# Performance work log

Hardware: AMD Instinct MI355X
Metric: run time of the kernel (lower is better)

The kernel has to match this reference:

```python
import jax, jax.numpy as jnp
import numpy as np

N, F_IN, F_OUT = 8192, 256, 128
ALPHA = 0.2  # LeakyReLU negative slope
NEG_INF = -9e15


def setup_inputs() -> dict:
    key = jax.random.key(0)
    k1, k2, k3, k4 = jax.random.split(key, 4)
    h = jax.random.normal(k1, (N, F_IN), dtype=jnp.float32)
    adj = jax.random.randint(k2, (N, N), 0, 2, dtype=jnp.int32)
    # Xavier-uniform-like init (gain=1.414)
    lim_w = 1.414 * np.sqrt(6.0 / (F_IN + F_OUT))
    W = jax.random.uniform(k3, (F_IN, F_OUT), dtype=jnp.float32, minval=-lim_w, maxval=lim_w)
    lim_a = 1.414 * np.sqrt(6.0 / (2 * F_OUT + 1))
    a = jax.random.uniform(k4, (2 * F_OUT, 1), dtype=jnp.float32, minval=-lim_a, maxval=lim_a)
    return {"h": h, "adj": adj, "W": W, "a": a}


def reference(h, adj, W, a):
    # Wh: [N, F_OUT]
    Wh = h @ W
    f_out = W.shape[1]
    # The torch code builds an [N, N, 2F] concat tensor; mathematically
    # e_ij = leakyrelu(a1 . Wh_i + a2 . Wh_j), so compute via two projections.
    a1 = a[:f_out, 0]   # [F_OUT]
    a2 = a[f_out:, 0]   # [F_OUT]
    f1 = Wh @ a1        # [N]
    f2 = Wh @ a2        # [N]
    e = jax.nn.leaky_relu(f1[:, None] + f2[None, :], negative_slope=ALPHA)  # [N, N]
    e = jnp.where(adj > 0, e, NEG_INF)
    attention = jax.nn.softmax(e, axis=1)  # [N, N]; dropout p=0 (eval mode)
    h_prime = attention @ Wh               # [N, F_OUT]
    return jax.nn.elu(h_prime)
```

## Files before the change

kernel.cpp:

```cpp
#include <hip/hip_runtime.h>
#include <hip/hip_bf16.h>
#include <math.h>

typedef short short8 __attribute__((ext_vector_type(8)));
typedef float f32x4 __attribute__((ext_vector_type(4)));
typedef int i32x4 __attribute__((ext_vector_type(4)));

#define NN 8192
#define FIN 256
#define FOUT 128
#define LRELU_A 0.2f
#define L2E 1.44269504088896f

__device__ __forceinline__ short f2bf(float x) {
    unsigned u = __builtin_bit_cast(unsigned, x);
    unsigned r = (u + 0x7FFFu + ((u >> 16) & 1u)) >> 16;
    return (short)r;
}

__device__ __forceinline__ short f2bf_fast(float x) {
    return __builtin_bit_cast(short, __float2bfloat16(x));
}

__global__ __launch_bounds__(256) void k_prep(const float* __restrict__ h,
                                              const float* __restrict__ W,
                                              const float* __restrict__ a,
                                              const int* __restrict__ adj,
                                              short* __restrict__ WhT,
                                              float* __restrict__ f1,
                                              float* __restrict__ f2,
                                              unsigned* __restrict__ packed) {
    __shared__ float hs[8][FIN];
    __shared__ unsigned char nib[2048];
    const int tid = threadIdx.x;
    const int bid = blockIdx.x;

    if (bid >= NN / 8) {
        const int row = bid - NN / 8;
        const i32x4* base = (const i32x4*)(adj + (size_t)row * NN);
        #pragma unroll
        for (int q = 0; q < 8; ++q) {
            int idx = q * 256 + tid;
            i32x4 v = __builtin_nontemporal_load(base + idx);
            unsigned b = (unsigned)(v.x & 1)        | ((unsigned)(v.y & 1) << 1) |
                         ((unsigned)(v.z & 1) << 2) | ((unsigned)(v.w & 1) << 3);
            nib[idx] = (unsigned char)b;
        }
        __syncthreads();
        unsigned long long n8 = *(const unsigned long long*)&nib[tid * 8];
        unsigned w = 0;
        #pragma unroll
        for (int j = 0; j < 8; ++j)
            w |= ((unsigned)((n8 >> (8 * j)) & 0xFull)) << (4 * j);
        packed[(size_t)row * (NN / 32) + tid] = w;
        return;
    }

    const int r0 = bid * 8;
    #pragma unroll
    for (int i = 0; i < 2; ++i) {
        int f4 = tid + 256 * i;
        int row = f4 >> 6;
        int k4 = (f4 & 63) << 2;
        *(float4*)&hs[row][k4] = *(const float4*)(h + (size_t)(r0 + row) * FIN + k4);
    }
    __syncthreads();
    const int c4 = (tid & 31) * 4;
    const int row = tid >> 5;
    float acc0 = 0.f, acc1 = 0.f, acc2 = 0.f, acc3 = 0.f;
    #pragma unroll 4
    for (int k = 0; k < FIN; ++k) {
        float hv = hs[row][k];
        float4 w4 = *(const float4*)(W + (size_t)k * FOUT + c4);
        acc0 = fmaf(hv, w4.x, acc0);
        acc1 = fmaf(hv, w4.y, acc1);
        acc2 = fmaf(hv, w4.z, acc2);
        acc3 = fmaf(hv, w4.w, acc3);
    }
    const int wr = r0 + row;
    WhT[(size_t)(c4 + 0) * NN + wr] = f2bf(acc0);
    WhT[(size_t)(c4 + 1) * NN + wr] = f2bf(acc1);
    WhT[(size_t)(c4 + 2) * NN + wr] = f2bf(acc2);
    WhT[(size_t)(c4 + 3) * NN + wr] = f2bf(acc3);

    float4 a1v = *(const float4*)(a + c4);
    float4 a2v = *(const float4*)(a + FOUT + c4);
    float p1 = acc0 * a1v.x + acc1 * a1v.y + acc2 * a1v.z + acc3 * a1v.w;
    float p2 = acc0 * a2v.x + acc1 * a2v.y + acc2 * a2v.z + acc3 * a2v.w;
    #pragma unroll
    for (int m = 1; m <= 16; m <<= 1) {
        p1 += __shfl_xor(p1, m, 64);
        p2 += __shfl_xor(p2, m, 64);
    }
    if ((tid & 31) == 0) {
        f1[wr] = p1;
        f2[wr] = p2;
    }
}

__global__ __launch_bounds__(256) void k_gmax(const float* __restrict__ f2,
                                              float* __restrict__ gmax) {
    const int tid = threadIdx.x;
    float m = -1e30f;
    for (int i = tid; i < NN; i += 256) m = fmaxf(m, f2[i]);
    #pragma unroll
    for (int s = 1; s <= 32; s <<= 1) m = fmaxf(m, __shfl_xor(m, s, 64));
    __shared__ float red[4];
    if ((tid & 63) == 0) red[tid >> 6] = m;
    __syncthreads();
    if (tid == 0) gmax[0] = fmaxf(fmaxf(red[0], red[1]), fmaxf(red[2], red[3]));
}

__device__ __forceinline__ void gat_body(const short* __restrict__ lrd, unsigned m8,
                                         float4 fa, float4 fb,
                                         float c1, float c2,
                                         f32x4 acc[9], short8 ones) {
    short8 b0 = *(const short8*)(lrd + 0 * 1024);
    short8 b1 = *(const short8*)(lrd + 1 * 1024);
    short8 b2 = *(const short8*)(lrd + 2 * 1024);
    short8 b3 = *(const short8*)(lrd + 3 * 1024);
    short8 b4 = *(const short8*)(lrd + 4 * 1024);
    short8 b5 = *(const short8*)(lrd + 5 * 1024);
    short8 b6 = *(const short8*)(lrd + 6 * 1024);
    short8 b7 = *(const short8*)(lrd + 7 * 1024);

    float fv[8] = {fa.x, fa.y, fa.z, fa.w, fb.x, fb.y, fb.z, fb.w};
    short8 af;
    #pragma unroll
    for (int i = 0; i < 8; ++i) {
        float u = fv[i] + c1;
        float v = fmaf(LRELU_A, fv[i], c2);
        float p = __builtin_amdgcn_exp2f(fmaxf(u, v));
        p = (m8 & (1u << i)) ? p : 0.0f;
        af[i] = f2bf_fast(p);
    }
    acc[0] = __builtin_amdgcn_mfma_f32_16x16x32_bf16(af, b0, acc[0], 0, 0, 0);
    acc[1] = __builtin_amdgcn_mfma_f32_16x16x32_bf16(af, b1, acc[1], 0, 0, 0);
    acc[2] = __builtin_amdgcn_mfma_f32_16x16x32_bf16(af, b2, acc[2], 0, 0, 0);
    acc[3] = __builtin_amdgcn_mfma_f32_16x16x32_bf16(af, b3, acc[3], 0, 0, 0);
    acc[4] = __builtin_amdgcn_mfma_f32_16x16x32_bf16(af, b4, acc[4], 0, 0, 0);
    acc[5] = __builtin_amdgcn_mfma_f32_16x16x32_bf16(af, b5, acc[5], 0, 0, 0);
    acc[6] = __builtin_amdgcn_mfma_f32_16x16x32_bf16(af, b6, acc[6], 0, 0, 0);
    acc[7] = __builtin_amdgcn_mfma_f32_16x16x32_bf16(af, b7, acc[7], 0, 0, 0);
    acc[8] = __builtin_amdgcn_mfma_f32_16x16x32_bf16(af, ones, acc[8], 0, 0, 0);
}

#define GAT_STEP(KOFF, MC, LRD0, LRD1, BUFW)                                       \
    {                                                                              \
        const int koff_ = (KOFF);                                                  \
        float4 fa0 = *(const float4*)(lf2 + koff_);                                \
        float4 fb0 = *(const float4*)(lf2 + koff_ + 4);                            \
        float4 fa1 = *(const float4*)(lf2 + koff_ + 32);                           \
        float4 fb1 = *(const float4*)(lf2 + koff_ + 36);                           \
        unsigned m0 = (MC.x >> mshift) & 0xffu;                                    \
        unsigned m1 = (MC.y >> mshift) & 0xffu;                                    \
        const int kpm_ = (koff_ + 128 < kchunk) ? koff_ + 128 : 0;                 \
        MC = *(const uint2*)(pkrow + (kpm_ >> 5));                                 \
        const int kst_ = (koff_ + 64 < kchunk) ? koff_ + 64 : 0;                   \
        short8 r0 = *(const short8*)(g00 + kst_);                                  \
        short8 r1 = *(const short8*)(g01 + kst_);                                  \
        short8 r2 = *(const short8*)(g10 + kst_);                                  \
        short8 r3 = *(const short8*)(g11 + kst_);                                  \
        gat_body(LRD0, m0, fa0, fb0, c1, c2, acc, ones);                           \
        gat_body(LRD1, m1, fa1, fb1, c1, c2, acc, ones);                           \
        *(short8*)((BUFW) + d00) = r0;                                             \
        *(short8*)((BUFW) + d01) = r1;                                             \
        *(short8*)((BUFW) + d10) = r2;                                             \
        *(short8*)((BUFW) + d11) = r3;                                             \
        asm volatile("s_waitcnt lgkmcnt(0)" ::: "memory");                         \
        __builtin_amdgcn_s_barrier();                                              \
    }

__global__ __launch_bounds__(256, 4) void k_attn(const unsigned* __restrict__ packed,
                                                 const short* __restrict__ WhT,
                                                 const float* __restrict__ f1,
                                                 const float* __restrict__ f2,
                                                 const float* __restrict__ gmax,
                                                 float* __restrict__ numb,
                                                 float* __restrict__ denb,
                                                 int kchunk, int nsplit) {
    __shared__ __align__(16) short ldsW[2][8192];
    __shared__ __align__(16) float ldsF2[2048];
    const int tid = threadIdx.x;
    const int lane = tid & 63;
    const int wave = tid >> 6;
    const int split = blockIdx.x & (nsplit - 1);
    const int rt = blockIdx.x / nsplit;
    const int rowbase = rt * 64 + wave * 16;
    const int col = lane & 15;
    const int kg = lane >> 4;
    const int arow = rowbase + col;

    const float f1r = f1[arow];
    const float gm = gmax[0];
    const float t0v = f1r + gm;
    const float mhat = fmaxf(t0v, LRELU_A * t0v);
    const float mh2 = mhat * L2E;
    const float c1 = fmaf(f1r, L2E, -mh2);
    const float c2 = fmaf(LRELU_A * f1r, L2E, -mh2);

    const short8 ones = {0x3F80, 0x3F80, 0x3F80, 0x3F80,
                         0x3F80, 0x3F80, 0x3F80, 0x3F80};

    const int kbase0 = split * kchunk;
    const unsigned* pkrow = packed + (size_t)arow * (NN / 32) + (kbase0 >> 5);
    const int mshift = kg * 8;
    const float* lf2 = ldsF2 + kg * 8;

    const int srow = wave * 32 + (lane >> 2);
    const int sx = srow & 7;
    const short* gsb = WhT + (size_t)srow * NN + kbase0 + (lane & 3) * 8;
    const short* g00 = gsb;
    const short* g01 = gsb + 32;
    const short* g10 = gsb + (size_t)16 * NN;
    const short* g11 = gsb + (size_t)16 * NN + 32;
    const int d00 = srow * 64        + ((((lane & 3) + 0) ^ sx) * 8);
    const int d01 = srow * 64        + ((((lane & 3) + 4) ^ sx) * 8);
    const int d10 = (srow + 16) * 64 + ((((lane & 3) + 0) ^ sx) * 8);
    const int d11 = (srow + 16) * 64 + ((((lane & 3) + 4) ^ sx) * 8);
    short* buf0 = &ldsW[0][0];
    short* buf1 = &ldsW[1][0];

    const short* lrdE0 = &ldsW[0][col * 64 + ((kg ^ (col & 7)) * 8)];
    const short* lrdE1 = &ldsW[0][col * 64 + (((kg ^ (col & 7)) * 8) ^ 32)];
    const short* lrdO0 = lrdE0 + 8192;
    const short* lrdO1 = lrdE1 + 8192;

    f32x4 acc[9] = {};

    for (int i = tid * 4; i < kchunk; i += 1024) {
        float4 v = *(const float4*)(f2 + kbase0 + i);
        v.x *= L2E; v.y *= L2E; v.z *= L2E; v.w *= L2E;
        *(float4*)&ldsF2[i] = v;
    }
    {
        short8 r0 = *(const short8*)(g00);
        short8 r1 = *(const short8*)(g01);
        short8 r2 = *(const short8*)(g10);
        short8 r3 = *(const short8*)(g11);
        *(short8*)(buf0 + d00) = r0;
        *(short8*)(buf0 + d01) = r1;
        *(short8*)(buf0 + d10) = r2;
        *(short8*)(buf0 + d11) = r3;
    }
    uint2 mA = *(const uint2*)(pkrow);
    uint2 mB = *(const uint2*)(pkrow + 2);
    asm volatile("s_waitcnt lgkmcnt(0)" ::: "memory");
    __builtin_amdgcn_s_barrier();

    for (int koff = 0; koff < kchunk; koff += 128) {
        GAT_STEP(koff,      mA, lrdE0, lrdE1, buf1);
        GAT_STEP(koff + 64, mB, lrdO0, lrdO1, buf0);
    }

    const int rsub = (lane >> 4) * 4;
    if (col == 0) {
        #pragma unroll
        for (int r = 0; r < 4; ++r)
            denb[(size_t)split * NN + rowbase + rsub + r] = acc[8][r];
    }

    float* np = numb + ((size_t)split * NN + rowbase) * FOUT;
    #pragma unroll
    for (int t = 0; t < 8; ++t) {
        #pragma unroll
        for (int r = 0; r < 4; ++r) {
            np[(size_t)(rsub + r) * FOUT + t * 16 + col] = acc[t][r];
        }
    }
}

__global__ __launch_bounds__(256) void k_final(const float* __restrict__ numb,
                                               const float* __restrict__ denb,
                                               float* __restrict__ out,
                                               int splitk) {
    const int idx = blockIdx.x * 256 + threadIdx.x;
    const int row = idx >> 7;
    float s = 0.0f, d = 0.0f;
    for (int sp = 0; sp < splitk; ++sp) {
        s += numb[((size_t)sp * NN) * FOUT + idx];
        d += denb[(size_t)sp * NN + row];
    }
    float v = s / d;
    out[idx] = v > 0.0f ? v : expm1f(v);
}

extern "C" void kernel_launch(void* const* d_in, const int* in_sizes, int n_in,
                              void* d_out, int out_size, void* d_ws, size_t ws_size,
                              hipStream_t stream) {
    const float* h = (const float*)d_in[0];
    const int* adj = (const int*)d_in[1];
    const float* W = (const float*)d_in[2];
    const float* a = (const float*)d_in[3];
    float* out = (float*)d_out;

    char* ws = (char*)d_ws;
    size_t off = 0;
    auto alloc = [&](size_t nbytes) {
        char* p = ws + off;
        off = (off + nbytes + 255) & ~(size_t)255;
        return p;
    };
    short* WhT     = (short*)alloc((size_t)FOUT * NN * 2);
    float* f1      = (float*)alloc(NN * 4);
    float* f2      = (float*)alloc(NN * 4);
    float* gmx     = (float*)alloc(256);
    unsigned* pkd  = (unsigned*)alloc((size_t)NN * (NN / 32) * 4);

    int splitk = 8;
    while (splitk > 1 &&
           off + (size_t)splitk * ((size_t)NN * FOUT * 4 + NN * 4 + 512) > ws_size)
        splitk >>= 1;
    float* numb = (float*)alloc((size_t)splitk * NN * FOUT * 4);
    float* denb = (float*)alloc((size_t)splitk * NN * 4);
    const int kchunk = NN / splitk;

    k_prep<<<NN / 8 + NN, 256, 0, stream>>>(h, W, a, adj, WhT, f1, f2, pkd);
    k_gmax<<<1, 256, 0, stream>>>(f2, gmx);
    k_attn<<<(NN / 64) * splitk, 256, 0, stream>>>(pkd, WhT, f1, f2, gmx, numb, denb,
                                                   kchunk, splitk);
    k_final<<<NN * FOUT / 256, 256, 0, stream>>>(numb, denb, out, splitk);
}
```

Measured before the change: 127.1 us.

## Stream WhT tiles via direct global-to-LDS loads and prefetch f2 from global

Replaces the register-staged copy of WhT tiles into shared memory with global_load_lds direct transfers, using a new XOR swizzle on the source address. The f2 values are no longer staged in LDS; each lane prefetches its own f2 and mask values from global memory one step ahead, with the log2e scaling folded into the FMAs. Synchronisation moves from lgkmcnt waits to vmcnt counting, and the B-fragment LDS reads are split into two groups to reduce register pressure. This aims to cut VGPR use and LDS store traffic, at the cost of a fragile vmcnt count and a swizzle that must match the reader's layout.

```diff
diff --git a/kernel.cpp b/kernel.cpp
--- a/kernel.cpp
+++ b/kernel.cpp
@@ -20,6 +20,12 @@
 
 __device__ __forceinline__ short f2bf_fast(float x) {
     return __builtin_bit_cast(short, __float2bfloat16(x));
+}
+
+__device__ __forceinline__ void gload_lds16(const void* g, void* l) {
+    __builtin_amdgcn_global_load_lds(
+        (const __attribute__((address_space(1))) void*)g,
+        (__attribute__((address_space(3))) void*)l, 16, 0, 0);
 }
 
 __global__ __launch_bounds__(256) void k_prep(const float* __restrict__ h,
@@ -115,59 +121,59 @@
                                          float4 fa, float4 fb,
                                          float c1, float c2,
                                          f32x4 acc[9], short8 ones) {
-    short8 b0 = *(const short8*)(lrd + 0 * 1024);
-    short8 b1 = *(const short8*)(lrd + 1 * 1024);
-    short8 b2 = *(const short8*)(lrd + 2 * 1024);
-    short8 b3 = *(const short8*)(lrd + 3 * 1024);
-    short8 b4 = *(const short8*)(lrd + 4 * 1024);
-    short8 b5 = *(const short8*)(lrd + 5 * 1024);
-    short8 b6 = *(const short8*)(lrd + 6 * 1024);
-    short8 b7 = *(const short8*)(lrd + 7 * 1024);
-
     float fv[8] = {fa.x, fa.y, fa.z, fa.w, fb.x, fb.y, fb.z, fb.w};
     short8 af;
     #pragma unroll
     for (int i = 0; i < 8; ++i) {
-        float u = fv[i] + c1;
-        float v = fmaf(LRELU_A, fv[i], c2);
+        float u = fmaf(L2E, fv[i], c1);
+        float v = fmaf(LRELU_A * L2E, fv[i], c2);
         float p = __builtin_amdgcn_exp2f(fmaxf(u, v));
         p = (m8 & (1u << i)) ? p : 0.0f;
         af[i] = f2bf_fast(p);
     }
-    acc[0] = __builtin_amdgcn_mfma_f32_16x16x32_bf16(af, b0, acc[0], 0, 0, 0);
-    acc[1] = __builtin_amdgcn_mfma_f32_16x16x32_bf16(af, b1, acc[1], 0, 0, 0);
-    acc[2] = __builtin_amdgcn_mfma_f32_16x16x32_bf16(af, b2, acc[2], 0, 0, 0);
-    acc[3] = __builtin_amdgcn_mfma_f32_16x16x32_bf16(af, b3, acc[3], 0, 0, 0);
-    acc[4] = __builtin_amdgcn_mfma_f32_16x16x32_bf16(af, b4, acc[4], 0, 0, 0);
-    acc[5] = __builtin_amdgcn_mfma_f32_16x16x32_bf16(af, b5, acc[5], 0, 0, 0);
-    acc[6] = __builtin_amdgcn_mfma_f32_16x16x32_bf16(af, b6, acc[6], 0, 0, 0);
-    acc[7] = __builtin_amdgcn_mfma_f32_16x16x32_bf16(af, b7, acc[7], 0, 0, 0);
+    {
+        short8 b0 = *(const short8*)(lrd + 0 * 1024);
+        short8 b1 = *(const short8*)(lrd + 1 * 1024);
+        short8 b2 = *(const short8*)(lrd + 2 * 1024);
+        short8 b3 = *(const short8*)(lrd + 3 * 1024);
+        acc[0] = __builtin_amdgcn_mfma_f32_16x16x32_bf16(af, b0, acc[0], 0, 0, 0);
+        acc[1] = __builtin_amdgcn_mfma_f32_16x16x32_bf16(af, b1, acc[1], 0, 0, 0);
+        acc[2] = __builtin_amdgcn_mfma_f32_16x16x32_bf16(af, b2, acc[2], 0, 0, 0);
+        acc[3] = __builtin_amdgcn_mfma_f32_16x16x32_bf16(af, b3, acc[3], 0, 0, 0);
+    }
+    {
+        short8 b4 = *(const short8*)(lrd + 4 * 1024);
+        short8 b5 = *(const short8*)(lrd + 5 * 1024);
+        short8 b6 = *(const short8*)(lrd + 6 * 1024);
+        short8 b7 = *(const short8*)(lrd + 7 * 1024);
+        acc[4] = __builtin_amdgcn_mfma_f32_16x16x32_bf16(af, b4, acc[4], 0, 0, 0);
+        acc[5] = __builtin_amdgcn_mfma_f32_16x16x32_bf16(af, b5, acc[5], 0, 0, 0);
+        acc[6] = __builtin_amdgcn_mfma_f32_16x16x32_bf16(af, b6, acc[6], 0, 0, 0);
+        acc[7] = __builtin_amdgcn_mfma_f32_16x16x32_bf16(af, b7, acc[7], 0, 0, 0);
+    }
     acc[8] = __builtin_amdgcn_mfma_f32_16x16x32_bf16(af, ones, acc[8], 0, 0, 0);
 }
 
-#define GAT_STEP(KOFF, MC, LRD0, LRD1, BUFW)                                       \
+#define GAT_STEP(KOFF, MC, FA0, FB0, FA1, FB1, LRD0, LRD1, LDST)                   \
     {                                                                              \
         const int koff_ = (KOFF);                                                  \
-        float4 fa0 = *(const float4*)(lf2 + koff_);                                \
-        float4 fb0 = *(const float4*)(lf2 + koff_ + 4);                            \
-        float4 fa1 = *(const float4*)(lf2 + koff_ + 32);                           \
-        float4 fb1 = *(const float4*)(lf2 + koff_ + 36);                           \
-        unsigned m0 = (MC.x >> mshift) & 0xffu;                                    \
-        unsigned m1 = (MC.y >> mshift) & 0xffu;                                    \
-        const int kpm_ = (koff_ + 128 < kchunk) ? koff_ + 128 : 0;                 \
-        MC = *(const uint2*)(pkrow + (kpm_ >> 5));                                 \
+        uint2 mc_ = MC;                                                            \
+        float4 fa0_ = FA0, fb0_ = FB0, fa1_ = FA1, fb1_ = FB1;                     \
         const int kst_ = (koff_ + 64 < kchunk) ? koff_ + 64 : 0;                   \
-        short8 r0 = *(const short8*)(g00 + kst_);                                  \
-        short8 r1 = *(const short8*)(g01 + kst_);                                  \
-        short8 r2 = *(const short8*)(g10 + kst_);                                  \
-        short8 r3 = *(const short8*)(g11 + kst_);                                  \
-        gat_body(LRD0, m0, fa0, fb0, c1, c2, acc, ones);                           \
-        gat_body(LRD1, m1, fa1, fb1, c1, c2, acc, ones);                           \
-        *(short8*)((BUFW) + d00) = r0;                                             \
-        *(short8*)((BUFW) + d01) = r1;                                             \
-        *(short8*)((BUFW) + d10) = r2;                                             \
-        *(short8*)((BUFW) + d11) = r3;                                             \
-        asm volatile("s_waitcnt lgkmcnt(0)" ::: "memory");                         \
+        gload_lds16(gsrc0 + kst_,           (LDST) + 0 * 512);                     \
+        gload_lds16(gsrc0 + kst_ + 8 * NN,  (LDST) + 1 * 512);                     \
+        gload_lds16(gsrc0 + kst_ + 16 * NN, (LDST) + 2 * 512);                     \
+        gload_lds16(gsrc0 + kst_ + 24 * NN, (LDST) + 3 * 512);                     \
+        const int kpf_ = (koff_ + 128 < kchunk) ? koff_ + 128 : 0;                 \
+        MC  = *(const uint2*)(pkrow + (kpf_ >> 5));                                \
+        FA0 = *(const float4*)(f2g + kpf_);                                        \
+        FB0 = *(const float4*)(f2g + kpf_ + 4);                                    \
+        FA1 = *(const float4*)(f2g + kpf_ + 32);                                   \
+        FB1 = *(const float4*)(f2g + kpf_ + 36);                                   \
+        __builtin_amdgcn_sched_barrier(0);                                         \
+        gat_body(LRD0, (mc_.x >> mshift) & 0xffu, fa0_, fb0_, c1, c2, acc, ones);  \
+        gat_body(LRD1, (mc_.y >> mshift) & 0xffu, fa1_, fb1_, c1, c2, acc, ones);  \
+        asm volatile("s_waitcnt vmcnt(5)" ::: "memory");                           \
         __builtin_amdgcn_s_barrier();                                              \
     }
 
@@ -180,7 +186,6 @@
                                                  float* __restrict__ denb,
                                                  int kchunk, int nsplit) {
     __shared__ __align__(16) short ldsW[2][8192];
-    __shared__ __align__(16) float ldsF2[2048];
     const int tid = threadIdx.x;
     const int lane = tid & 63;
     const int wave = tid >> 6;
@@ -205,21 +210,13 @@
     const int kbase0 = split * kchunk;
     const unsigned* pkrow = packed + (size_t)arow * (NN / 32) + (kbase0 >> 5);
     const int mshift = kg * 8;
-    const float* lf2 = ldsF2 + kg * 8;
-
-    const int srow = wave * 32 + (lane >> 2);
-    const int sx = srow & 7;
-    const short* gsb = WhT + (size_t)srow * NN + kbase0 + (lane & 3) * 8;
-    const short* g00 = gsb;
-    const short* g01 = gsb + 32;
-    const short* g10 = gsb + (size_t)16 * NN;
-    const short* g11 = gsb + (size_t)16 * NN + 32;
-    const int d00 = srow * 64        + ((((lane & 3) + 0) ^ sx) * 8);
-    const int d01 = srow * 64        + ((((lane & 3) + 4) ^ sx) * 8);
-    const int d10 = (srow + 16) * 64 + ((((lane & 3) + 0) ^ sx) * 8);
-    const int d11 = (srow + 16) * 64 + ((((lane & 3) + 4) ^ sx) * 8);
-    short* buf0 = &ldsW[0][0];
-    short* buf1 = &ldsW[1][0];
+    const float* f2g = f2 + kbase0 + kg * 8;
+
+    const int sr = lane >> 3;
+    const short* gsrc0 = WhT + (size_t)(wave * 32 + sr) * NN + kbase0 +
+                         (((lane & 7) ^ sr) * 8);
+    short* ldstE = &ldsW[0][wave * 2048];
+    short* ldstO = &ldsW[1][wave * 2048];
 
     const short* lrdE0 = &ldsW[0][col * 64 + ((kg ^ (col & 7)) * 8)];
     const short* lrdE1 = &ldsW[0][col * 64 + (((kg ^ (col & 7)) * 8) ^ 32)];
@@ -228,29 +225,26 @@
 
     f32x4 acc[9] = {};
 
-    for (int i = tid * 4; i < kchunk; i += 1024) {
-        float4 v = *(const float4*)(f2 + kbase0 + i);
-        v.x *= L2E; v.y *= L2E; v.z *= L2E; v.w *= L2E;
-        *(float4*)&ldsF2[i] = v;
-    }
-    {
-        short8 r0 = *(const short8*)(g00);
-        short8 r1 = *(const short8*)(g01);
-        short8 r2 = *(const short8*)(g10);
-        short8 r3 = *(const short8*)(g11);
-        *(short8*)(buf0 + d00) = r0;
-        *(short8*)(buf0 + d01) = r1;
-        *(short8*)(buf0 + d10) = r2;
-        *(short8*)(buf0 + d11) = r3;
-    }
-    uint2 mA = *(const uint2*)(pkrow);
-    uint2 mB = *(const uint2*)(pkrow + 2);
-    asm volatile("s_waitcnt lgkmcnt(0)" ::: "memory");
+    gload_lds16(gsrc0,           ldstE + 0 * 512);
+    gload_lds16(gsrc0 + 8 * NN,  ldstE + 1 * 512);
+    gload_lds16(gsrc0 + 16 * NN, ldstE + 2 * 512);
+    gload_lds16(gsrc0 + 24 * NN, ldstE + 3 * 512);
+    uint2  mE  = *(const uint2*)(pkrow);
+    float4 fE0 = *(const float4*)(f2g);
+    float4 fE1 = *(const float4*)(f2g + 4);
+    float4 fE2 = *(const float4*)(f2g + 32);
+    float4 fE3 = *(const float4*)(f2g + 36);
+    uint2  mO  = *(const uint2*)(pkrow + 2);
+    float4 fO0 = *(const float4*)(f2g + 64);
+    float4 fO1 = *(const float4*)(f2g + 68);
+    float4 fO2 = *(const float4*)(f2g + 96);
+    float4 fO3 = *(const float4*)(f2g + 100);
+    asm volatile("s_waitcnt vmcnt(10)" ::: "memory");
     __builtin_amdgcn_s_barrier();
 
     for (int koff = 0; koff < kchunk; koff += 128) {
-        GAT_STEP(koff,      mA, lrdE0, lrdE1, buf1);
-        GAT_STEP(koff + 64, mB, lrdO0, lrdO1, buf0);
+        GAT_STEP(koff,      mE, fE0, fE1, fE2, fE3, lrdE0, lrdE1, ldstO);
+        GAT_STEP(koff + 64, mO, fO0, fO1, fO2, fO3, lrdO0, lrdO1, ldstE);
     }
 
     const int rsub = (lane >> 4) * 4;
```

New measurement: 128.3 us. About the same (+0.9%).

## Fuse global max and split-K reduction into attention kernel via semaphore

Applied to the files above, without the earlier changes.

Removes the separate gmax and final-reduction kernels. Each attention block now computes the f2 max redundantly from global memory, and the last split block per row tile, detected with an atomic counter, reduces the numerator and denominator partials and applies ELU. The L2E scaling moves into the fma inside the exp path. This cuts two launches and a tail kernel, at the cost of a redundant 32KB read per block and a serialized reduction done by the last-arriving block.

```diff
diff --git a/kernel.cpp b/kernel.cpp
--- a/kernel.cpp
+++ b/kernel.cpp
@@ -29,7 +29,8 @@
                                               short* __restrict__ WhT,
                                               float* __restrict__ f1,
                                               float* __restrict__ f2,
-                                              unsigned* __restrict__ packed) {
+                                              unsigned* __restrict__ packed,
+                                              int* __restrict__ sem) {
     __shared__ float hs[8][FIN];
     __shared__ unsigned char nib[2048];
     const int tid = threadIdx.x;
@@ -56,6 +57,8 @@
         return;
     }
 
+    if (bid == 0 && tid < NN / 64) sem[tid] = 0;
+
     const int r0 = bid * 8;
     #pragma unroll
     for (int i = 0; i < 2; ++i) {
@@ -96,19 +99,6 @@
         f1[wr] = p1;
         f2[wr] = p2;
     }
-}
-
-__global__ __launch_bounds__(256) void k_gmax(const float* __restrict__ f2,
-                                              float* __restrict__ gmax) {
-    const int tid = threadIdx.x;
-    float m = -1e30f;
-    for (int i = tid; i < NN; i += 256) m = fmaxf(m, f2[i]);
-    #pragma unroll
-    for (int s = 1; s <= 32; s <<= 1) m = fmaxf(m, __shfl_xor(m, s, 64));
-    __shared__ float red[4];
-    if ((tid & 63) == 0) red[tid >> 6] = m;
-    __syncthreads();
-    if (tid == 0) gmax[0] = fmaxf(fmaxf(red[0], red[1]), fmaxf(red[2], red[3]));
 }
 
 __device__ __forceinline__ void gat_body(const short* __restrict__ lrd, unsigned m8,
@@ -128,8 +118,8 @@
     short8 af;
     #pragma unroll
     for (int i = 0; i < 8; ++i) {
-        float u = fv[i] + c1;
-        float v = fmaf(LRELU_A, fv[i], c2);
+        float u = fmaf(L2E, fv[i], c1);
+        float v = fmaf(LRELU_A * L2E, fv[i], c2);
         float p = __builtin_amdgcn_exp2f(fmaxf(u, v));
         p = (m8 & (1u << i)) ? p : 0.0f;
         af[i] = f2bf_fast(p);
@@ -175,9 +165,10 @@
                                                  const short* __restrict__ WhT,
                                                  const float* __restrict__ f1,
                                                  const float* __restrict__ f2,
-                                                 const float* __restrict__ gmax,
                                                  float* __restrict__ numb,
                                                  float* __restrict__ denb,
+                                                 float* __restrict__ out,
+                                                 int* __restrict__ sem,
                                                  int kchunk, int nsplit) {
     __shared__ __align__(16) short ldsW[2][8192];
     __shared__ __align__(16) float ldsF2[2048];
@@ -191,8 +182,19 @@
     const int kg = lane >> 4;
     const int arow = rowbase + col;
 
+    float gm = -3.4e38f;
+    for (int i = tid * 4; i < NN; i += 1024) {
+        float4 v = *(const float4*)(f2 + i);
+        gm = fmaxf(fmaxf(gm, fmaxf(v.x, v.y)), fmaxf(v.z, v.w));
+    }
+    #pragma unroll
+    for (int s = 1; s <= 32; s <<= 1) gm = fmaxf(gm, __shfl_xor(gm, s, 64));
+    if (lane == 0) ldsF2[wave] = gm;
+    __syncthreads();
+    gm = fmaxf(fmaxf(ldsF2[0], ldsF2[1]), fmaxf(ldsF2[2], ldsF2[3]));
+    __syncthreads();
+
     const float f1r = f1[arow];
-    const float gm = gmax[0];
     const float t0v = f1r + gm;
     const float mhat = fmaxf(t0v, LRELU_A * t0v);
     const float mh2 = mhat * L2E;
@@ -228,11 +230,8 @@
 
     f32x4 acc[9] = {};
 
-    for (int i = tid * 4; i < kchunk; i += 1024) {
-        float4 v = *(const float4*)(f2 + kbase0 + i);
-        v.x *= L2E; v.y *= L2E; v.z *= L2E; v.w *= L2E;
-        *(float4*)&ldsF2[i] = v;
-    }
+    for (int i = tid * 4; i < kchunk; i += 1024)
+        *(float4*)&ldsF2[i] = *(const float4*)(f2 + kbase0 + i);
     {
         short8 r0 = *(const short8*)(g00);
         short8 r1 = *(const short8*)(g01);
@@ -259,7 +258,6 @@
         for (int r = 0; r < 4; ++r)
             denb[(size_t)split * NN + rowbase + rsub + r] = acc[8][r];
     }
-
     float* np = numb + ((size_t)split * NN + rowbase) * FOUT;
     #pragma unroll
     for (int t = 0; t < 8; ++t) {
@@ -268,21 +266,33 @@
             np[(size_t)(rsub + r) * FOUT + t * 16 + col] = acc[t][r];
         }
     }
-}
-
-__global__ __launch_bounds__(256) void k_final(const float* __restrict__ numb,
-                                               const float* __restrict__ denb,
-                                               float* __restrict__ out,
-                                               int splitk) {
-    const int idx = blockIdx.x * 256 + threadIdx.x;
-    const int row = idx >> 7;
-    float s = 0.0f, d = 0.0f;
-    for (int sp = 0; sp < splitk; ++sp) {
-        s += numb[((size_t)sp * NN) * FOUT + idx];
-        d += denb[(size_t)sp * NN + row];
-    }
-    float v = s / d;
-    out[idx] = v > 0.0f ? v : expm1f(v);
+
+    __threadfence();
+    __syncthreads();
+    int* flag = (int*)&ldsF2[64];
+    if (tid == 0) flag[0] = (atomicAdd(&sem[rt], 1) == nsplit - 1);
+    __syncthreads();
+    if (!flag[0]) return;
+    __threadfence();
+
+    const int rowbase0 = rt * 64;
+    float* dsum = (float*)ldsF2;
+    for (int i = tid; i < 64; i += 256) {
+        float d = 0.0f;
+        for (int sp = 0; sp < nsplit; ++sp)
+            d += denb[(size_t)sp * NN + rowbase0 + i];
+        dsum[i] = d;
+    }
+    __syncthreads();
+    for (int i = tid; i < 64 * FOUT; i += 256) {
+        const int r = i >> 7;
+        const int c = i & (FOUT - 1);
+        float s = 0.0f;
+        for (int sp = 0; sp < nsplit; ++sp)
+            s += numb[((size_t)sp * NN + rowbase0 + r) * FOUT + c];
+        float v = s / dsum[r];
+        out[(size_t)(rowbase0 + r) * FOUT + c] = v > 0.0f ? v : expm1f(v);
+    }
 }
 
 extern "C" void kernel_launch(void* const* d_in, const int* in_sizes, int n_in,
@@ -304,8 +314,8 @@
     short* WhT     = (short*)alloc((size_t)FOUT * NN * 2);
     float* f1      = (float*)alloc(NN * 4);
     float* f2      = (float*)alloc(NN * 4);
-    float* gmx     = (float*)alloc(256);
     unsigned* pkd  = (unsigned*)alloc((size_t)NN * (NN / 32) * 4);
+    int* sem       = (int*)alloc((NN / 64) * 4);
 
     int splitk = 8;
     while (splitk > 1 &&
@@ -315,9 +325,7 @@
     float* denb = (float*)alloc((size_t)splitk * NN * 4);
     const int kchunk = NN / splitk;
 
-    k_prep<<<NN / 8 + NN, 256, 0, stream>>>(h, W, a, adj, WhT, f1, f2, pkd);
-    k_gmax<<<1, 256, 0, stream>>>(f2, gmx);
-    k_attn<<<(NN / 64) * splitk, 256, 0, stream>>>(pkd, WhT, f1, f2, gmx, numb, denb,
-                                                   kchunk, splitk);
-    k_final<<<NN * FOUT / 256, 256, 0, stream>>>(numb, denb, out, splitk);
-}
+    k_prep<<<NN / 8 + NN, 256, 0, stream>>>(h, W, a, adj, WhT, f1, f2, pkd, sem);
+    k_attn<<<(NN / 64) * splitk, 256, 0, stream>>>(pkd, WhT, f1, f2, numb, denb,
+                                                   out, sem, kchunk, splitk);
+}
```

New measurement: 377.3 us. 197% more time.
